# Optimization experiments

Hardware: AMD Instinct MI355X
Metric: run time of the kernel (lower is better)

## Reference

```python
import jax, jax.numpy as jnp
import numpy as np

DIM = 1024
HEADS = 16
HEAD_DIM = DIM // HEADS
SCALE = HEAD_DIM ** -0.5
B, N = 2, 2048


def setup_inputs() -> dict:
    key = jax.random.key(0)
    ks = jax.random.split(key, 12)
    s = DIM ** -0.5
    return {
        "x_real": jax.random.normal(ks[0], (B, N, DIM), jnp.float32),
        "x_imag": jax.random.normal(ks[1], (B, N, DIM), jnp.float32),
        "Wqkv_r": jax.random.normal(ks[2], (3 * DIM, DIM), jnp.float32) * s,
        "bqkv_r": jax.random.normal(ks[3], (3 * DIM,), jnp.float32) * 0.01,
        "Wqkv_i": jax.random.normal(ks[4], (3 * DIM, DIM), jnp.float32) * s,
        "bqkv_i": jax.random.normal(ks[5], (3 * DIM,), jnp.float32) * 0.01,
        "Wout_r": jax.random.normal(ks[6], (DIM, DIM), jnp.float32) * s,
        "bout_r": jax.random.normal(ks[7], (DIM,), jnp.float32) * 0.01,
        "Wout_i": jax.random.normal(ks[8], (DIM, DIM), jnp.float32) * s,
        "bout_i": jax.random.normal(ks[9], (DIM,), jnp.float32) * 0.01,
    }


def _split_heads(qkv):
    # (B, N, 3*D) -> q, k, v each (B, H, N, hd)
    b, n, _ = qkv.shape
    qkv = qkv.reshape(b, n, 3, HEADS, HEAD_DIM).transpose(2, 0, 3, 1, 4)
    return qkv[0], qkv[1], qkv[2]


def reference(x_real, x_imag, Wqkv_r, bqkv_r, Wqkv_i, bqkv_i,
              Wout_r, bout_r, Wout_i, bout_i):
    b, n, d = x_real.shape
    q_r, k_r, v_r = _split_heads(x_real @ Wqkv_r.T + bqkv_r)
    q_i, k_i, v_i = _split_heads(x_imag @ Wqkv_i.T + bqkv_i)

    # complex score: (q_r + i q_i) (k_r - i k_i)^T pattern per source
    attn_real = (jnp.einsum('bhqd,bhkd->bhqk', q_r, k_r)
                 + jnp.einsum('bhqd,bhkd->bhqk', q_i, k_i)) * SCALE
    attn_imag = (jnp.einsum('bhqd,bhkd->bhqk', q_i, k_r)
                 - jnp.einsum('bhqd,bhkd->bhqk', q_r, k_i)) * SCALE
    attn_mag = jnp.sqrt(attn_real ** 2 + attn_imag ** 2)
    w = jax.nn.softmax(attn_mag, axis=-1)

    out_r = jnp.einsum('bhqk,bhkd->bhqd', w, v_r).transpose(0, 2, 1, 3).reshape(b, n, d)
    out_i = jnp.einsum('bhqk,bhkd->bhqd', w, v_i).transpose(0, 2, 1, 3).reshape(b, n, d)
    out_r = out_r @ Wout_r.T + bout_r
    out_i = out_i @ Wout_i.T + bout_i
    return out_r, out_i
```

## Files before the change

### kernel.cpp

```cpp
#include <hip/hip_runtime.h>


#define DIM_   1024
#define HEADS_ 16
#define HD_    64
#define BB_    2
#define NN_    2048
#define MTOT_  (BB_*NN_)
#define SCALE_ 0.125f

typedef __bf16 bf16;
typedef __bf16 bf16x8 __attribute__((ext_vector_type(8)));
typedef short  s16x8  __attribute__((ext_vector_type(8)));
typedef float  fx4    __attribute__((ext_vector_type(4)));

__device__ __forceinline__ bf16x8 neg8(bf16x8 v) {
    s16x8 s;
    __builtin_memcpy(&s, &v, sizeof(s));
    s ^= (short)0x8000;
    bf16x8 r;
    __builtin_memcpy(&r, &s, sizeof(r));
    return r;
}

__device__ __forceinline__ void gl_lds16(const void* g, void* l) {
    __builtin_amdgcn_global_load_lds(
        (const __attribute__((address_space(1))) unsigned int*)g,
        (__attribute__((address_space(3))) unsigned int*)l, 16, 0, 0);
}

#define PIPE_SYNC() asm volatile("s_waitcnt vmcnt(2)\n\ts_barrier" ::: "memory")

__global__ __launch_bounds__(256) void cvt_prepass(
    const float* __restrict__ xr, const float* __restrict__ xi,
    const float* __restrict__ wqr, const float* __restrict__ wqi,
    const float* __restrict__ wor, const float* __restrict__ woi,
    bf16* __restrict__ xbf, bf16* __restrict__ wqkv, bf16* __restrict__ wout)
{
    const int bid = blockIdx.x;
    const float* src; bf16* dst; int rel;
    if      (bid < 2048) { src = xr;  dst = xbf;           rel = bid; }
    else if (bid < 4096) { src = xi;  dst = xbf + 4194304; rel = bid - 2048; }
    else if (bid < 5632) { src = wqr; dst = wqkv;          rel = bid - 4096; }
    else if (bid < 7168) { src = wqi; dst = wqkv + 3145728; rel = bid - 5632; }
    else if (bid < 7680) { src = wor; dst = wout;          rel = bid - 7168; }
    else                 { src = woi; dst = wout + 1048576; rel = bid - 7680; }
    size_t base = (size_t)rel * 2048 + (size_t)threadIdx.x * 8;
    fx4 a = *(const fx4*)(src + base);
    fx4 b = *(const fx4*)(src + base + 4);
    bf16x8 o;
#pragma unroll
    for (int j = 0; j < 4; ++j) { o[j] = (bf16)a[j]; o[j+4] = (bf16)b[j]; }
    *(bf16x8*)(dst + base) = o;
}

#define GEMM_CORE(Aptr, Bptr)                                                  \
    __shared__ __align__(16) bf16 As[128*64];                                  \
    __shared__ __align__(16) bf16 Bs[128*64];                                  \
    const int tid  = threadIdx.x;                                              \
    const int w    = tid >> 6, lane = tid & 63;                                \
    const int quad = lane >> 4, lc = lane & 15;                                \
    const int wm   = (w >> 1) * 64, wn = (w & 1) * 64;                         \
    const int rj   = lane >> 3;                                                \
    const int sc   = (lane & 7) ^ rj;                                          \
    const fx4 fzero = {0.f, 0.f, 0.f, 0.f};                                    \
    fx4 acc[4][4];                                                             \
    _Pragma("unroll")                                                          \
    for (int mi = 0; mi < 4; ++mi)                                             \
        _Pragma("unroll")                                                      \
        for (int ni = 0; ni < 4; ++ni) acc[mi][ni] = fzero;                    \
    for (int k0 = 0; k0 < DIM_; k0 += 64) {                                    \
        _Pragma("unroll")                                                      \
        for (int j = 0; j < 4; ++j) {                                          \
            int grp = j*4 + w;                                                 \
            int gr  = grp*8 + rj;                                              \
            gl_lds16(Aptr + (size_t)(m0+gr)*DIM_ + k0 + sc*8, As + grp*512);   \
            gl_lds16(Bptr + (size_t)(n0+gr)*DIM_ + k0 + sc*8, Bs + grp*512);   \
        }                                                                      \
        __syncthreads();                                                       \
        bf16x8 af[2][4], bfr[2][4];                                            \
        _Pragma("unroll")                                                      \
        for (int ks = 0; ks < 2; ++ks) {                                       \
            _Pragma("unroll")                                                  \
            for (int mi = 0; mi < 4; ++mi)                                     \
                af[ks][mi] = *(bf16x8*)&As[(wm+mi*16+lc)*64 + (((ks*4+quad)^(lc&7))*8)]; \
            _Pragma("unroll")                                                  \
            for (int ni = 0; ni < 4; ++ni)                                     \
                bfr[ks][ni] = *(bf16x8*)&Bs[(wn+ni*16+lc)*64 + (((ks*4+quad)^(lc&7))*8)]; \
        }                                                                      \
        _Pragma("unroll")                                                      \
        for (int ks = 0; ks < 2; ++ks)                                         \
            _Pragma("unroll")                                                  \
            for (int mi = 0; mi < 4; ++mi)                                     \
                _Pragma("unroll")                                              \
                for (int ni = 0; ni < 4; ++ni)                                 \
                    acc[mi][ni] = __builtin_amdgcn_mfma_f32_16x16x32_bf16(     \
                        af[ks][mi], bfr[ks][ni], acc[mi][ni], 0, 0, 0);        \
        __syncthreads();                                                       \
    }

__global__ __launch_bounds__(256) void qkv_gemm_dma(
    const bf16* __restrict__ xbf, const bf16* __restrict__ wqkv,
    const float* __restrict__ br, const float* __restrict__ bi,
    bf16* __restrict__ qbuf, bf16* __restrict__ kbuf, bf16* __restrict__ vbuf)
{
    const int z = blockIdx.z;
    const bf16* __restrict__ Ap = xbf  + (size_t)z * 4194304;
    const bf16* __restrict__ Bp = wqkv + (size_t)z * 3145728;
    const float* __restrict__ bias = z ? bi : br;
    const int n0 = blockIdx.x * 128;
    const int m0 = blockIdx.y * 128;

    GEMM_CORE(Ap, Bp)

#pragma unroll
    for (int mi = 0; mi < 4; ++mi)
#pragma unroll
        for (int ni = 0; ni < 4; ++ni)
#pragma unroll
            for (int r = 0; r < 4; ++r) {
                int gm = m0 + wm + mi*16 + quad*4 + r;
                int gc = n0 + wn + ni*16 + lc;
                float val = acc[mi][ni][r] + bias[gc];
                bf16 bv = (bf16)val;
                int which = gc >> 10, h = (gc >> 6) & 15, hd = gc & 63;
                int b = gm >> 11, n = gm & 2047;
                size_t base = (size_t)((z*BB_ + b)*HEADS_ + h);
                if (which == 0)      qbuf[(base*NN_ + n)*HD_ + hd] = bv;
                else if (which == 1) kbuf[(base*NN_ + n)*HD_ + hd] = bv;
                else                 vbuf[(base*HD_ + hd)*NN_ + n] = bv;
            }
}

__global__ __launch_bounds__(256) void out_gemm_dma(
    const bf16* __restrict__ obuf, const bf16* __restrict__ wout,
    const float* __restrict__ br, const float* __restrict__ bi,
    float* __restrict__ out)
{
    const int z = blockIdx.z;
    const bf16* __restrict__ Ap = obuf + (size_t)z * 4194304;
    const bf16* __restrict__ Bp = wout + (size_t)z * 1048576;
    const float* __restrict__ bias = z ? bi : br;
    float* __restrict__ dst = out + (size_t)z * 4194304;
    const int n0 = blockIdx.x * 128;
    const int m0 = blockIdx.y * 128;

    GEMM_CORE(Ap, Bp)

#pragma unroll
    for (int mi = 0; mi < 4; ++mi)
#pragma unroll
        for (int ni = 0; ni < 4; ++ni)
#pragma unroll
            for (int r = 0; r < 4; ++r) {
                int gm = m0 + wm + mi*16 + quad*4 + r;
                int gc = n0 + wn + ni*16 + lc;
                dst[(size_t)gm*DIM_ + gc] = acc[mi][ni][r] + bias[gc];
            }
}

#define KT 32
#define NSTEP (NN_/KT)

__global__ __launch_bounds__(512, 4) void attn_fwd(
    const bf16* __restrict__ qbuf, const bf16* __restrict__ kbuf,
    const bf16* __restrict__ vbuf, bf16* __restrict__ obuf)
{
    const int bid = blockIdx.x;
    const int xcd = bid & 7;
    const int loc = bid >> 3;
    const int hb  = xcd*4 + (loc >> 4);
    const int blk = loc & 15;
    const int b = hb >> 4, h = hb & 15;

    const int tid  = threadIdx.x;
    const int w    = tid >> 6, lane = tid & 63;
    const int quad = lane >> 4, lc = lane & 15;
    const int q0   = blk*128 + w*16;

    __shared__ __align__(16) bf16 KV[3*8192];

    const size_t hR = (size_t)(b)*HEADS_ + h;
    const size_t hI = (size_t)(BB_ + b)*HEADS_ + h;
    const bf16* qrg = qbuf + hR*NN_*HD_;
    const bf16* qig = qbuf + hI*NN_*HD_;
    const char* krg = (const char*)(kbuf + hR*NN_*HD_);
    const char* kig = (const char*)(kbuf + hI*NN_*HD_);
    const char* vrg = (const char*)(vbuf + hR*HD_*NN_);
    const char* vig = (const char*)(vbuf + hI*HD_*NN_);

    const bf16* pr = qrg + (size_t)(q0 + lc)*HD_ + quad*8;
    const bf16* pi = qig + (size_t)(q0 + lc)*HD_ + quad*8;
    bf16x8 qr0 = *(const bf16x8*)(pr);
    bf16x8 qr1 = *(const bf16x8*)(pr + 32);
    bf16x8 qi0 = *(const bf16x8*)(pi);
    bf16x8 qi1 = *(const bf16x8*)(pi + 32);
    bf16x8 nqr0 = neg8(qr0), nqr1 = neg8(qr1);

    const int arr = w >> 1, half = w & 1;
    const char* stg_base = (arr == 0) ? krg : (arr == 1) ? kig
                         : (arr == 2) ? vrg : vig;
    size_t lane_off, step_mul, j_mul;
    if (arr < 2) {
        const int rl = lane >> 3;
        const int p0 = (rl >> 2)*8 + half*4 + (rl & 3);
        lane_off = (size_t)p0*128 + (size_t)((lane & 7) ^ rl)*16;
        step_mul = 4096;  j_mul = 2048;
    } else {
        lane_off = (size_t)half*131072
                 + (size_t)(lane >> 2)*4096 + (size_t)((lane & 3) ^ ((lane >> 3) & 3))*16;
        step_mul = 64;    j_mul = 65536;
    }
    const char* stg0 = stg_base + lane_off;
    const int lds_base = arr*2048 + half*1024;

    int koff[2][2], voff[4];
#pragma unroll
    for (int kb = 0; kb < 2; ++kb)
#pragma unroll
        for (int hf = 0; hf < 2; ++hf) {
            int r = kb*16 + lc;
            koff[kb][hf] = r*64 + (((hf*4 + quad) ^ (r & 7))*8);
        }
#pragma unroll
    for (int vb = 0; vb < 4; ++vb) {
        int r = vb*16 + lc;
        voff[vb] = r*32 + ((quad ^ ((r >> 1) & 3))*8);
    }

    const fx4 fzero = {0.f, 0.f, 0.f, 0.f};
    fx4 O[2][4];
    float l_ = 0.f;
#pragma unroll
    for (int ri = 0; ri < 2; ++ri)
#pragma unroll
        for (int vb = 0; vb < 4; ++vb) O[ri][vb] = fzero;
    bf16x8 pf = {};
    bf16x8 vf[2][4];

    const float CEXP = SCALE_ * 1.44269504f;

    {
        bf16* l = KV + lds_base;
        gl_lds16(stg0,          l);
        gl_lds16(stg0 + j_mul,  l + 512);
        l = KV + 8192 + lds_base;
        gl_lds16(stg0 + step_mul,         l);
        gl_lds16(stg0 + step_mul + j_mul, l + 512);
    }
    PIPE_SYNC();

    int b0 = 0, b1 = 8192, b2 = 16384;
    for (int s = 0; s < NSTEP; ++s) {
        if (s < NSTEP-2) {
            const char* g = stg0 + (size_t)(s+2)*step_mul;
            bf16* l = KV + b2 + lds_base;
            gl_lds16(g,         l);
            gl_lds16(g + j_mul, l + 512);
        }

        if (s > 0) {
#pragma unroll
            for (int ri = 0; ri < 2; ++ri)
#pragma unroll
                for (int vb = 0; vb < 4; ++vb)
                    O[ri][vb] = __builtin_amdgcn_mfma_f32_16x16x32_bf16(
                        pf, vf[ri][vb], O[ri][vb], 0, 0, 0);
        }

        bf16x8 kr_[2][2], ki_[2][2];
#pragma unroll
        for (int kb = 0; kb < 2; ++kb)
#pragma unroll
            for (int hf = 0; hf < 2; ++hf) {
                kr_[kb][hf] = *(bf16x8*)&KV[b0 + koff[kb][hf]];
                ki_[kb][hf] = *(bf16x8*)&KV[b0 + 2048 + koff[kb][hf]];
            }

#pragma unroll
        for (int kb = 0; kb < 2; ++kb) {
            fx4 sr = fzero, si = fzero;
            sr = __builtin_amdgcn_mfma_f32_16x16x32_bf16(kr_[kb][0], qr0,  sr, 0,0,0);
            sr = __builtin_amdgcn_mfma_f32_16x16x32_bf16(kr_[kb][1], qr1,  sr, 0,0,0);
            sr = __builtin_amdgcn_mfma_f32_16x16x32_bf16(ki_[kb][0], qi0,  sr, 0,0,0);
            sr = __builtin_amdgcn_mfma_f32_16x16x32_bf16(ki_[kb][1], qi1,  sr, 0,0,0);
            si = __builtin_amdgcn_mfma_f32_16x16x32_bf16(kr_[kb][0], qi0,  si, 0,0,0);
            si = __builtin_amdgcn_mfma_f32_16x16x32_bf16(kr_[kb][1], qi1,  si, 0,0,0);
            si = __builtin_amdgcn_mfma_f32_16x16x32_bf16(ki_[kb][0], nqr0, si, 0,0,0);
            si = __builtin_amdgcn_mfma_f32_16x16x32_bf16(ki_[kb][1], nqr1, si, 0,0,0);
#pragma unroll
            for (int r4 = 0; r4 < 4; ++r4) {
                float s2 = sr[r4]*sr[r4] + si[r4]*si[r4];
                float mg = __builtin_amdgcn_sqrtf(s2);
                float pv = __builtin_amdgcn_exp2f(mg * CEXP);
                l_ += pv;
                pf[kb*4 + r4] = (bf16)pv;
            }
        }

#pragma unroll
        for (int ri = 0; ri < 2; ++ri)
#pragma unroll
            for (int vb = 0; vb < 4; ++vb)
                vf[ri][vb] = *(bf16x8*)&KV[b0 + (2+ri)*2048 + voff[vb]];

        PIPE_SYNC();
        int t = b0; b0 = b1; b1 = b2; b2 = t;
    }

#pragma unroll
    for (int ri = 0; ri < 2; ++ri)
#pragma unroll
        for (int vb = 0; vb < 4; ++vb)
            O[ri][vb] = __builtin_amdgcn_mfma_f32_16x16x32_bf16(
                pf, vf[ri][vb], O[ri][vb], 0, 0, 0);

    l_ += __shfl_xor(l_, 16);
    l_ += __shfl_xor(l_, 32);
    float inv[4];
#pragma unroll
    for (int r = 0; r < 4; ++r) inv[r] = 1.f / __shfl(l_, quad*4 + r);

    bf16* obr = obuf + ((size_t)(b)*NN_)*DIM_;
    bf16* obi = obuf + ((size_t)(BB_ + b)*NN_)*DIM_;
#pragma unroll
    for (int vb = 0; vb < 4; ++vb)
#pragma unroll
        for (int r = 0; r < 4; ++r) {
            int gn = q0 + quad*4 + r;
            int gc = h*HD_ + vb*16 + lc;
            obr[(size_t)gn*DIM_ + gc] = (bf16)(O[0][vb][r] * inv[r]);
            obi[(size_t)gn*DIM_ + gc] = (bf16)(O[1][vb][r] * inv[r]);
        }
}

__global__ __launch_bounds__(256) void qkv_gemm_legacy(
    const float* __restrict__ xr, const float* __restrict__ xi,
    const float* __restrict__ Wr, const float* __restrict__ Wi,
    const float* __restrict__ br, const float* __restrict__ bi,
    bf16* __restrict__ qbuf, bf16* __restrict__ kbuf, bf16* __restrict__ vbuf)
{
    const int z = blockIdx.z;
    const float* __restrict__ A    = z ? xi : xr;
    const float* __restrict__ W    = z ? Wi : Wr;
    const float* __restrict__ bias = z ? bi : br;
    const int n0 = blockIdx.x * 128;
    const int m0 = blockIdx.y * 128;

    __shared__ bf16 As[128*40];
    __shared__ bf16 Bs[128*40];

    const int tid  = threadIdx.x;
    const int w    = tid >> 6, lane = tid & 63;
    const int quad = lane >> 4, lc = lane & 15;
    const int wm   = (w >> 1) * 64, wn = (w & 1) * 64;

    const fx4 fzero = {0.f, 0.f, 0.f, 0.f};
    fx4 acc[4][4];
#pragma unroll
    for (int mi = 0; mi < 4; ++mi)
#pragma unroll
        for (int ni = 0; ni < 4; ++ni) acc[mi][ni] = fzero;

    for (int k0 = 0; k0 < DIM_; k0 += 32) {
#pragma unroll
        for (int it = 0; it < 2; ++it) {
            int flat = it*2048 + tid*8;
            int row = flat >> 5, col = flat & 31;
            const float* pa = A + (size_t)(m0+row)*DIM_ + k0 + col;
            const float* pb = W + (size_t)(n0+row)*DIM_ + k0 + col;
            fx4 a0 = *(const fx4*)pa, a1 = *(const fx4*)(pa+4);
            fx4 b0 = *(const fx4*)pb, b1 = *(const fx4*)(pb+4);
            bf16x8 av, bv;
#pragma unroll
            for (int j = 0; j < 4; ++j) {
                av[j] = (bf16)a0[j]; av[j+4] = (bf16)a1[j];
                bv[j] = (bf16)b0[j]; bv[j+4] = (bf16)b1[j];
            }
            *(bf16x8*)&As[row*40 + col] = av;
            *(bf16x8*)&Bs[row*40 + col] = bv;
        }
        __syncthreads();

        bf16x8 af[4], bfr[4];
#pragma unroll
        for (int mi = 0; mi < 4; ++mi) af[mi]  = *(bf16x8*)&As[(wm + mi*16 + lc)*40 + quad*8];
#pragma unroll
        for (int ni = 0; ni < 4; ++ni) bfr[ni] = *(bf16x8*)&Bs[(wn + ni*16 + lc)*40 + quad*8];
#pragma unroll
        for (int mi = 0; mi < 4; ++mi)
#pragma unroll
            for (int ni = 0; ni < 4; ++ni)
                acc[mi][ni] = __builtin_amdgcn_mfma_f32_16x16x32_bf16(af[mi], bfr[ni], acc[mi][ni], 0, 0, 0);
        __syncthreads();
    }

#pragma unroll
    for (int mi = 0; mi < 4; ++mi)
#pragma unroll
        for (int ni = 0; ni < 4; ++ni)
#pragma unroll
            for (int r = 0; r < 4; ++r) {
                int gm = m0 + wm + mi*16 + quad*4 + r;
                int gc = n0 + wn + ni*16 + lc;
                float val = acc[mi][ni][r] + bias[gc];
                bf16 bv = (bf16)val;
                int which = gc >> 10, h = (gc >> 6) & 15, hd = gc & 63;
                int b = gm >> 11, n = gm & 2047;
                size_t base = (size_t)((z*BB_ + b)*HEADS_ + h);
                if (which == 0)      qbuf[(base*NN_ + n)*HD_ + hd] = bv;
                else if (which == 1) kbuf[(base*NN_ + n)*HD_ + hd] = bv;
                else                 vbuf[(base*HD_ + hd)*NN_ + n] = bv;
            }
}

__global__ __launch_bounds__(256) void out_gemm_legacy(
    const bf16* __restrict__ obuf,
    const float* __restrict__ Wr, const float* __restrict__ Wi,
    const float* __restrict__ br, const float* __restrict__ bi,
    float* __restrict__ out)
{
    const int z = blockIdx.z;
    const bf16*  __restrict__ A    = obuf + (size_t)z * MTOT_ * DIM_;
    const float* __restrict__ W    = z ? Wi : Wr;
    const float* __restrict__ bias = z ? bi : br;
    float* __restrict__ dst        = out + (size_t)z * MTOT_ * DIM_;
    const int n0 = blockIdx.x * 128;
    const int m0 = blockIdx.y * 128;

    __shared__ bf16 As[128*40];
    __shared__ bf16 Bs[128*40];

    const int tid  = threadIdx.x;
    const int w    = tid >> 6, lane = tid & 63;
    const int quad = lane >> 4, lc = lane & 15;
    const int wm   = (w >> 1) * 64, wn = (w & 1) * 64;

    const fx4 fzero = {0.f, 0.f, 0.f, 0.f};
    fx4 acc[4][4];
#pragma unroll
    for (int mi = 0; mi < 4; ++mi)
#pragma unroll
        for (int ni = 0; ni < 4; ++ni) acc[mi][ni] = fzero;

    for (int k0 = 0; k0 < DIM_; k0 += 32) {
#pragma unroll
        for (int it = 0; it < 2; ++it) {
            int flat = it*2048 + tid*8;
            int row = flat >> 5, col = flat & 31;
            *(bf16x8*)&As[row*40 + col] = *(const bf16x8*)(A + (size_t)(m0+row)*DIM_ + k0 + col);
            const float* pb = W + (size_t)(n0+row)*DIM_ + k0 + col;
            fx4 b0 = *(const fx4*)pb, b1 = *(const fx4*)(pb+4);
            bf16x8 bv;
#pragma unroll
            for (int j = 0; j < 4; ++j) { bv[j] = (bf16)b0[j]; bv[j+4] = (bf16)b1[j]; }
            *(bf16x8*)&Bs[row*40 + col] = bv;
        }
        __syncthreads();

        bf16x8 af[4], bfr[4];
#pragma unroll
        for (int mi = 0; mi < 4; ++mi) af[mi]  = *(bf16x8*)&As[(wm + mi*16 + lc)*40 + quad*8];
#pragma unroll
        for (int ni = 0; ni < 4; ++ni) bfr[ni] = *(bf16x8*)&Bs[(wn + ni*16 + lc)*40 + quad*8];
#pragma unroll
        for (int mi = 0; mi < 4; ++mi)
#pragma unroll
            for (int ni = 0; ni < 4; ++ni)
                acc[mi][ni] = __builtin_amdgcn_mfma_f32_16x16x32_bf16(af[mi], bfr[ni], acc[mi][ni], 0, 0, 0);
        __syncthreads();
    }

#pragma unroll
    for (int mi = 0; mi < 4; ++mi)
#pragma unroll
        for (int ni = 0; ni < 4; ++ni)
#pragma unroll
            for (int r = 0; r < 4; ++r) {
                int gm = m0 + wm + mi*16 + quad*4 + r;
                int gc = n0 + wn + ni*16 + lc;
                dst[(size_t)gm*DIM_ + gc] = acc[mi][ni][r] + bias[gc];
            }
}

extern "C" void kernel_launch(void* const* d_in, const int* in_sizes, int n_in,
                              void* d_out, int out_size, void* d_ws, size_t ws_size,
                              hipStream_t stream) {
    const float* xr  = (const float*)d_in[0];
    const float* xi  = (const float*)d_in[1];
    const float* Wqr = (const float*)d_in[2];
    const float* bqr = (const float*)d_in[3];
    const float* Wqi = (const float*)d_in[4];
    const float* bqi = (const float*)d_in[5];
    const float* Wor = (const float*)d_in[6];
    const float* bor = (const float*)d_in[7];
    const float* Woi = (const float*)d_in[8];
    const float* boi = (const float*)d_in[9];
    float* out = (float*)d_out;

    bf16* ws = (bf16*)d_ws;
    const size_t NEED = 83886080ull;

    if (ws_size >= NEED) {
        bf16* xbf  = ws;
        bf16* wqkv = ws + 8388608;
        bf16* wout = ws + 14680064;
        bf16* qb   = ws + 16777216;
        bf16* kb   = ws + 25165824;
        bf16* vb   = ws + 33554432;
        bf16* obuf = xbf;

        cvt_prepass<<<dim3(8192), 256, 0, stream>>>(xr, xi, Wqr, Wqi, Wor, Woi,
                                                    xbf, wqkv, wout);
        qkv_gemm_dma<<<dim3(24, 32, 2), 256, 0, stream>>>(xbf, wqkv, bqr, bqi,
                                                          qb, kb, vb);
        attn_fwd<<<dim3(512), 512, 0, stream>>>(qb, kb, vb, obuf);
        out_gemm_dma<<<dim3(8, 32, 2), 256, 0, stream>>>(obuf, wout, bor, boi, out);
    } else {
        const size_t per = (size_t)2 * BB_ * HEADS_ * NN_ * HD_;
        bf16* qb   = ws;
        bf16* kb   = ws + per;
        bf16* vb   = ws + 2*per;
        bf16* obuf = ws + 3*per;
        qkv_gemm_legacy<<<dim3(24, 32, 2), 256, 0, stream>>>(xr, xi, Wqr, Wqi,
                                                             bqr, bqi, qb, kb, vb);
        attn_fwd<<<dim3(512), 512, 0, stream>>>(qb, kb, vb, obuf);
        out_gemm_legacy<<<dim3(8, 32, 2), 256, 0, stream>>>(obuf, Wor, Woi,
                                                            bor, boi, out);
    }
}
```

Before: 337.5 us.

## Process two query tiles per warp in attention with 256-thread blocks

Each attention warp now computes 32 query rows instead of 16, reusing every K/V fragment read from LDS for two query tiles. The block shrinks to 4 warps, each staging one of the K-real/K-imag/V-real/V-imag arrays with four async loads per step, and wait counts are adjusted accordingly. The imaginary-score negation is moved from q to the shared k fragments. This cuts LDS traffic and barrier participants per query, at the cost of higher register pressure and fewer resident waves for latency hiding.

Measured after the change: 350.3 us. 1.04x slower.

```diff
diff --git a/kernel.cpp b/kernel.cpp
--- a/kernel.cpp
+++ b/kernel.cpp
@@ -28,8 +28,6 @@
         (const __attribute__((address_space(1))) unsigned int*)g,
         (__attribute__((address_space(3))) unsigned int*)l, 16, 0, 0);
 }
-
-#define PIPE_SYNC() asm volatile("s_waitcnt vmcnt(2)\n\ts_barrier" ::: "memory")
 
 __global__ __launch_bounds__(256) void cvt_prepass(
     const float* __restrict__ xr, const float* __restrict__ xi,
@@ -162,7 +160,10 @@
 #define KT 32
 #define NSTEP (NN_/KT)
 
-__global__ __launch_bounds__(512, 4) void attn_fwd(
+#define PIPE_SYNC4() asm volatile("s_waitcnt vmcnt(4)\n\ts_barrier" ::: "memory")
+#define FULL_SYNC()  asm volatile("s_waitcnt vmcnt(0)\n\ts_barrier" ::: "memory")
+
+__global__ __launch_bounds__(256, 2) void attn_fwd(
     const bf16* __restrict__ qbuf, const bf16* __restrict__ kbuf,
     const bf16* __restrict__ vbuf, bf16* __restrict__ obuf)
 {
@@ -176,7 +177,7 @@
     const int tid  = threadIdx.x;
     const int w    = tid >> 6, lane = tid & 63;
     const int quad = lane >> 4, lc = lane & 15;
-    const int q0   = blk*128 + w*16;
+    const int q0   = blk*128 + w*32;
 
     __shared__ __align__(16) bf16 KV[3*8192];
 
@@ -189,30 +190,36 @@
     const char* vrg = (const char*)(vbuf + hR*HD_*NN_);
     const char* vig = (const char*)(vbuf + hI*HD_*NN_);
 
-    const bf16* pr = qrg + (size_t)(q0 + lc)*HD_ + quad*8;
-    const bf16* pi = qig + (size_t)(q0 + lc)*HD_ + quad*8;
-    bf16x8 qr0 = *(const bf16x8*)(pr);
-    bf16x8 qr1 = *(const bf16x8*)(pr + 32);
-    bf16x8 qi0 = *(const bf16x8*)(pi);
-    bf16x8 qi1 = *(const bf16x8*)(pi + 32);
-    bf16x8 nqr0 = neg8(qr0), nqr1 = neg8(qr1);
-
-    const int arr = w >> 1, half = w & 1;
+    bf16x8 qr[2][2], qi[2][2];
+#pragma unroll
+    for (int qh = 0; qh < 2; ++qh) {
+        const bf16* pr = qrg + (size_t)(q0 + qh*16 + lc)*HD_ + quad*8;
+        const bf16* pi = qig + (size_t)(q0 + qh*16 + lc)*HD_ + quad*8;
+        qr[qh][0] = *(const bf16x8*)(pr);
+        qr[qh][1] = *(const bf16x8*)(pr + 32);
+        qi[qh][0] = *(const bf16x8*)(pi);
+        qi[qh][1] = *(const bf16x8*)(pi + 32);
+    }
+
+    const int arr = w;
     const char* stg_base = (arr == 0) ? krg : (arr == 1) ? kig
                          : (arr == 2) ? vrg : vig;
-    size_t lane_off, step_mul, j_mul;
+    size_t lane_off, step_mul;
+    int g1, g2, g3;
     if (arr < 2) {
         const int rl = lane >> 3;
-        const int p0 = (rl >> 2)*8 + half*4 + (rl & 3);
+        const int p0 = (rl >> 2)*8 + (rl & 3);
         lane_off = (size_t)p0*128 + (size_t)((lane & 7) ^ rl)*16;
-        step_mul = 4096;  j_mul = 2048;
+        step_mul = 4096;  g1 = 2048; g2 = 512; g3 = 2560;
     } else {
-        lane_off = (size_t)half*131072
-                 + (size_t)(lane >> 2)*4096 + (size_t)((lane & 3) ^ ((lane >> 3) & 3))*16;
-        step_mul = 64;    j_mul = 65536;
+        lane_off = (size_t)(lane >> 2)*4096 + (size_t)((lane & 3) ^ ((lane >> 3) & 3))*16;
+        step_mul = 64;    g1 = 65536; g2 = 131072; g3 = 196608;
     }
     const char* stg0 = stg_base + lane_off;
-    const int lds_base = arr*2048 + half*1024;
+    const int lds_base = arr*2048;
+
+#define STAGE4(gp, lp) do { gl_lds16((gp), (lp)); gl_lds16((gp)+g1, (lp)+512); \
+                            gl_lds16((gp)+g2, (lp)+1024); gl_lds16((gp)+g3, (lp)+1536); } while (0)
 
     int koff[2][2], voff[4];
 #pragma unroll
@@ -229,43 +236,39 @@
     }
 
     const fx4 fzero = {0.f, 0.f, 0.f, 0.f};
-    fx4 O[2][4];
-    float l_ = 0.f;
-#pragma unroll
-    for (int ri = 0; ri < 2; ++ri)
-#pragma unroll
-        for (int vb = 0; vb < 4; ++vb) O[ri][vb] = fzero;
-    bf16x8 pf = {};
+    fx4 O[2][2][4];
+    float l_[2] = {0.f, 0.f};
+#pragma unroll
+    for (int qh = 0; qh < 2; ++qh)
+#pragma unroll
+        for (int ri = 0; ri < 2; ++ri)
+#pragma unroll
+            for (int vb = 0; vb < 4; ++vb) O[qh][ri][vb] = fzero;
+    bf16x8 pf[2] = {};
     bf16x8 vf[2][4];
 
     const float CEXP = SCALE_ * 1.44269504f;
 
-    {
-        bf16* l = KV + lds_base;
-        gl_lds16(stg0,          l);
-        gl_lds16(stg0 + j_mul,  l + 512);
-        l = KV + 8192 + lds_base;
-        gl_lds16(stg0 + step_mul,         l);
-        gl_lds16(stg0 + step_mul + j_mul, l + 512);
-    }
-    PIPE_SYNC();
+    STAGE4(stg0,            KV + lds_base);
+    STAGE4(stg0 + step_mul, KV + 8192 + lds_base);
+    PIPE_SYNC4();
 
     int b0 = 0, b1 = 8192, b2 = 16384;
     for (int s = 0; s < NSTEP; ++s) {
         if (s < NSTEP-2) {
             const char* g = stg0 + (size_t)(s+2)*step_mul;
-            bf16* l = KV + b2 + lds_base;
-            gl_lds16(g,         l);
-            gl_lds16(g + j_mul, l + 512);
+            STAGE4(g, KV + b2 + lds_base);
         }
 
         if (s > 0) {
 #pragma unroll
-            for (int ri = 0; ri < 2; ++ri)
-#pragma unroll
-                for (int vb = 0; vb < 4; ++vb)
-                    O[ri][vb] = __builtin_amdgcn_mfma_f32_16x16x32_bf16(
-                        pf, vf[ri][vb], O[ri][vb], 0, 0, 0);
+            for (int qh = 0; qh < 2; ++qh)
+#pragma unroll
+                for (int ri = 0; ri < 2; ++ri)
+#pragma unroll
+                    for (int vb = 0; vb < 4; ++vb)
+                        O[qh][ri][vb] = __builtin_amdgcn_mfma_f32_16x16x32_bf16(
+                            pf[qh], vf[ri][vb], O[qh][ri][vb], 0, 0, 0);
         }
 
         bf16x8 kr_[2][2], ki_[2][2];
@@ -279,22 +282,27 @@
 
 #pragma unroll
         for (int kb = 0; kb < 2; ++kb) {
-            fx4 sr = fzero, si = fzero;
-            sr = __builtin_amdgcn_mfma_f32_16x16x32_bf16(kr_[kb][0], qr0,  sr, 0,0,0);
-            sr = __builtin_amdgcn_mfma_f32_16x16x32_bf16(kr_[kb][1], qr1,  sr, 0,0,0);
-            sr = __builtin_amdgcn_mfma_f32_16x16x32_bf16(ki_[kb][0], qi0,  sr, 0,0,0);
-            sr = __builtin_amdgcn_mfma_f32_16x16x32_bf16(ki_[kb][1], qi1,  sr, 0,0,0);
-            si = __builtin_amdgcn_mfma_f32_16x16x32_bf16(kr_[kb][0], qi0,  si, 0,0,0);
-            si = __builtin_amdgcn_mfma_f32_16x16x32_bf16(kr_[kb][1], qi1,  si, 0,0,0);
-            si = __builtin_amdgcn_mfma_f32_16x16x32_bf16(ki_[kb][0], nqr0, si, 0,0,0);
-            si = __builtin_amdgcn_mfma_f32_16x16x32_bf16(ki_[kb][1], nqr1, si, 0,0,0);
-#pragma unroll
-            for (int r4 = 0; r4 < 4; ++r4) {
-                float s2 = sr[r4]*sr[r4] + si[r4]*si[r4];
-                float mg = __builtin_amdgcn_sqrtf(s2);
-                float pv = __builtin_amdgcn_exp2f(mg * CEXP);
-                l_ += pv;
-                pf[kb*4 + r4] = (bf16)pv;
+            bf16x8 nki0 = neg8(ki_[kb][0]);
+            bf16x8 nki1 = neg8(ki_[kb][1]);
+#pragma unroll
+            for (int qh = 0; qh < 2; ++qh) {
+                fx4 sr = fzero, si = fzero;
+                sr = __builtin_amdgcn_mfma_f32_16x16x32_bf16(kr_[kb][0], qr[qh][0], sr, 0,0,0);
+                sr = __builtin_amdgcn_mfma_f32_16x16x32_bf16(kr_[kb][1], qr[qh][1], sr, 0,0,0);
+                sr = __builtin_amdgcn_mfma_f32_16x16x32_bf16(ki_[kb][0], qi[qh][0], sr, 0,0,0);
+                sr = __builtin_amdgcn_mfma_f32_16x16x32_bf16(ki_[kb][1], qi[qh][1], sr, 0,0,0);
+                si = __builtin_amdgcn_mfma_f32_16x16x32_bf16(kr_[kb][0], qi[qh][0], si, 0,0,0);
+                si = __builtin_amdgcn_mfma_f32_16x16x32_bf16(kr_[kb][1], qi[qh][1], si, 0,0,0);
+                si = __builtin_amdgcn_mfma_f32_16x16x32_bf16(nki0,       qr[qh][0], si, 0,0,0);
+                si = __builtin_amdgcn_mfma_f32_16x16x32_bf16(nki1,       qr[qh][1], si, 0,0,0);
+#pragma unroll
+                for (int r4 = 0; r4 < 4; ++r4) {
+                    float s2 = sr[r4]*sr[r4] + si[r4]*si[r4];
+                    float mg = __builtin_amdgcn_sqrtf(s2);
+                    float pv = __builtin_amdgcn_exp2f(mg * CEXP);
+                    l_[qh] += pv;
+                    pf[qh][kb*4 + r4] = (bf16)pv;
+                }
             }
         }
 
@@ -304,34 +312,41 @@
             for (int vb = 0; vb < 4; ++vb)
                 vf[ri][vb] = *(bf16x8*)&KV[b0 + (2+ri)*2048 + voff[vb]];
 
-        PIPE_SYNC();
+        if (s == NSTEP-2) FULL_SYNC();
+        else              PIPE_SYNC4();
         int t = b0; b0 = b1; b1 = b2; b2 = t;
     }
 
 #pragma unroll
-    for (int ri = 0; ri < 2; ++ri)
-#pragma unroll
-        for (int vb = 0; vb < 4; ++vb)
-            O[ri][vb] = __builtin_amdgcn_mfma_f32_16x16x32_bf16(
-                pf, vf[ri][vb], O[ri][vb], 0, 0, 0);
-
-    l_ += __shfl_xor(l_, 16);
-    l_ += __shfl_xor(l_, 32);
-    float inv[4];
-#pragma unroll
-    for (int r = 0; r < 4; ++r) inv[r] = 1.f / __shfl(l_, quad*4 + r);
+    for (int qh = 0; qh < 2; ++qh)
+#pragma unroll
+        for (int ri = 0; ri < 2; ++ri)
+#pragma unroll
+            for (int vb = 0; vb < 4; ++vb)
+                O[qh][ri][vb] = __builtin_amdgcn_mfma_f32_16x16x32_bf16(
+                    pf[qh], vf[ri][vb], O[qh][ri][vb], 0, 0, 0);
 
     bf16* obr = obuf + ((size_t)(b)*NN_)*DIM_;
     bf16* obi = obuf + ((size_t)(BB_ + b)*NN_)*DIM_;
 #pragma unroll
-    for (int vb = 0; vb < 4; ++vb)
-#pragma unroll
-        for (int r = 0; r < 4; ++r) {
-            int gn = q0 + quad*4 + r;
-            int gc = h*HD_ + vb*16 + lc;
-            obr[(size_t)gn*DIM_ + gc] = (bf16)(O[0][vb][r] * inv[r]);
-            obi[(size_t)gn*DIM_ + gc] = (bf16)(O[1][vb][r] * inv[r]);
-        }
+    for (int qh = 0; qh < 2; ++qh) {
+        float lq = l_[qh];
+        lq += __shfl_xor(lq, 16);
+        lq += __shfl_xor(lq, 32);
+        float inv[4];
+#pragma unroll
+        for (int r = 0; r < 4; ++r) inv[r] = 1.f / __shfl(lq, quad*4 + r);
+#pragma unroll
+        for (int vb = 0; vb < 4; ++vb)
+#pragma unroll
+            for (int r = 0; r < 4; ++r) {
+                int gn = q0 + qh*16 + quad*4 + r;
+                int gc = h*HD_ + vb*16 + lc;
+                obr[(size_t)gn*DIM_ + gc] = (bf16)(O[qh][0][vb][r] * inv[r]);
+                obi[(size_t)gn*DIM_ + gc] = (bf16)(O[qh][1][vb][r] * inv[r]);
+            }
+    }
+#undef STAGE4
 }
 
 __global__ __launch_bounds__(256) void qkv_gemm_legacy(
@@ -514,7 +529,7 @@
                                                     xbf, wqkv, wout);
         qkv_gemm_dma<<<dim3(24, 32, 2), 256, 0, stream>>>(xbf, wqkv, bqr, bqi,
                                                           qb, kb, vb);
-        attn_fwd<<<dim3(512), 512, 0, stream>>>(qb, kb, vb, obuf);
+        attn_fwd<<<dim3(512), 256, 0, stream>>>(qb, kb, vb, obuf);
         out_gemm_dma<<<dim3(8, 32, 2), 256, 0, stream>>>(obuf, wout, bor, boi, out);
     } else {
         const size_t per = (size_t)2 * BB_ * HEADS_ * NN_ * HD_;
@@ -524,7 +539,7 @@
         bf16* obuf = ws + 3*per;
         qkv_gemm_legacy<<<dim3(24, 32, 2), 256, 0, stream>>>(xr, xi, Wqr, Wqi,
                                                              bqr, bqi, qb, kb, vb);
-        attn_fwd<<<dim3(512), 512, 0, stream>>>(qb, kb, vb, obuf);
+        attn_fwd<<<dim3(512), 256, 0, stream>>>(qb, kb, vb, obuf);
         out_gemm_legacy<<<dim3(8, 32, 2), 256, 0, stream>>>(obuf, Wor, Woi,
                                                             bor, boi, out);
     }
```
